# Performance work log

Measured on AMD Instinct MI355X. Metric: run time of the kernel, lower is better.

The kernel has to match this reference:

```python
import jax, jax.numpy as jnp
import numpy as np
from jax import lax

E = 3  # num_experts

def _maxpool2(x):
    return lax.reduce_window(x, -jnp.inf, lax.max, (1, 1, 2, 2), (1, 1, 2, 2), 'VALID')

def _mixed_conv(x, experts, routing, stride, pad):
    # per-sample expert-mixed convolution via grouped conv trick
    B, Ci, H, W = x.shape
    _, Co, _, k, _ = experts.shape
    kern = jnp.einsum('be,eoikl->boikl', routing, experts).reshape(B * Co, Ci, k, k)
    y = lax.conv_general_dilated(
        x.reshape(1, B * Ci, H, W), kern, (stride, stride),
        [(pad, pad), (pad, pad)],
        dimension_numbers=('NCHW', 'OIHW', 'NCHW'),
        feature_group_count=B)
    return y.reshape(B, Co, y.shape[2], y.shape[3])

def _dyres_conv(x, experts, rw, rb, stride=1, pad=1):
    # DyRes mode 'A': routing from avg-pool + spatial-std descriptors, softmax over experts
    avg = x.mean((2, 3))
    std = x.std((2, 3))
    r = jax.nn.softmax((avg + std) @ rw.T + rb, axis=-1)  # [B, E]
    return _mixed_conv(x, experts, r, stride, pad)

def _cond_conv(x, experts, rw, rb, stride=1, pad=1):
    # CondConv: sigmoid routing from global average pool
    r = jax.nn.sigmoid(x.mean((2, 3)) @ rw.T + rb)  # [B, E]
    return _mixed_conv(x, experts, r, stride, pad)

def _conv_init(key, co, ci, k):
    return jax.random.normal(key, (E, co, ci, k, k), jnp.float32) * np.sqrt(2.0 / (ci * k * k)).astype(np.float32)

def setup_inputs() -> dict:
    key = jax.random.key(0)
    ks = jax.random.split(key, 20)
    B = 512
    d = {}
    d['x'] = jax.random.normal(ks[0], (B, 3, 32, 32), jnp.float32)
    d['dw1'] = _conv_init(ks[1], 64, 3, 3)
    d['rw1'] = jax.random.normal(ks[2], (E, 3), jnp.float32) * 0.1
    d['rb1'] = jnp.zeros((E,), jnp.float32)
    d['dw2'] = _conv_init(ks[3], 192, 64, 3)
    d['rw2'] = jax.random.normal(ks[4], (E, 64), jnp.float32) * 0.1
    d['rb2'] = jnp.zeros((E,), jnp.float32)
    d['dw3'] = _conv_init(ks[5], 384, 192, 3)
    d['rw3'] = jax.random.normal(ks[6], (E, 192), jnp.float32) * 0.1
    d['rb3'] = jnp.zeros((E,), jnp.float32)
    d['cw4'] = _conv_init(ks[7], 256, 384, 3)
    d['cr4w'] = jax.random.normal(ks[8], (E, 384), jnp.float32) * 0.1
    d['cr4b'] = jnp.zeros((E,), jnp.float32)
    d['cw5'] = _conv_init(ks[9], 256, 256, 3)
    d['cr5w'] = jax.random.normal(ks[10], (E, 256), jnp.float32) * 0.1
    d['cr5b'] = jnp.zeros((E,), jnp.float32)
    d['fw1'] = jax.random.normal(ks[11], (4096, 1024), jnp.float32) * np.sqrt(2.0 / 1024).astype(np.float32)
    d['fb1'] = jnp.zeros((4096,), jnp.float32)
    d['fw2'] = jax.random.normal(ks[12], (4096, 4096), jnp.float32) * np.sqrt(2.0 / 4096).astype(np.float32)
    d['fb2'] = jnp.zeros((4096,), jnp.float32)
    d['fw3'] = jax.random.normal(ks[13], (100, 4096), jnp.float32) * np.sqrt(1.0 / 4096).astype(np.float32)
    d['fb3'] = jnp.zeros((100,), jnp.float32)
    return d

def reference(x, dw1, rw1, rb1, dw2, rw2, rb2, dw3, rw3, rb3,
              cw4, cr4w, cr4b, cw5, cr5w, cr5b,
              fw1, fb1, fw2, fb2, fw3, fb3):
    h = jax.nn.relu(_dyres_conv(x, dw1, rw1, rb1, stride=2))   # [B,64,16,16]
    h = _maxpool2(h)                                           # [B,64,8,8]
    h = jax.nn.relu(_dyres_conv(h, dw2, rw2, rb2))             # [B,192,8,8]
    h = _maxpool2(h)                                           # [B,192,4,4]
    h = jax.nn.relu(_dyres_conv(h, dw3, rw3, rb3))             # [B,384,4,4]
    h = jax.nn.relu(_cond_conv(h, cw4, cr4w, cr4b))            # [B,256,4,4]
    h = jax.nn.relu(_cond_conv(h, cw5, cr5w, cr5b))            # [B,256,4,4]
    h = _maxpool2(h)                                           # [B,256,2,2]
    h = h.reshape(h.shape[0], -1)                              # [B,1024]
    h = jax.nn.relu(h @ fw1.T + fb1)
    h = jax.nn.relu(h @ fw2.T + fb2)
    return h @ fw3.T + fb3                                     # [B,100]
```

## Files before the change

kernel.cpp:

```cpp
#include <hip/hip_runtime.h>
#include <math.h>


typedef unsigned short u16;
typedef unsigned int u32;
typedef short bf16x8 __attribute__((ext_vector_type(8)));
typedef float f32x4 __attribute__((ext_vector_type(4)));

__device__ __forceinline__ u16 bf16_rne(float f) {
    u32 u = __float_as_uint(f);
    return (u16)((u + 0x7fffu + ((u >> 16) & 1u)) >> 16);
}
__device__ __forceinline__ u32 packsplit(float v) {
    u16 h = bf16_rne(v);
    float hf = __uint_as_float((u32)h << 16);
    u16 l = bf16_rne(v - hf);
    return ((u32)h << 16) | l;
}
__device__ __forceinline__ float unpackf(u32 p) {
    return __uint_as_float(p & 0xffff0000u) + __uint_as_float(p << 16);
}
__device__ __forceinline__ int xcd_swz(int bid, int n) {
    if ((n & 7) != 0) return bid;
    int cpx = n >> 3;
    return (bid & 7) * cpx + (bid >> 3);
}

__global__ __launch_bounds__(256)
void wsplit_kernel(const float* __restrict__ W, u16* __restrict__ whi,
                   u16* __restrict__ wlo, int total, int Kper, int Kpad)
{
    int idx = blockIdx.x * 256 + threadIdx.x;
    if (idx >= total) return;
    int r = idx / Kpad, k = idx - r * Kpad;
    float v = (k < Kper) ? W[(size_t)r * Kper + k] : 0.f;
    u16 h = bf16_rne(v);
    whi[idx] = h;
    wlo[idx] = bf16_rne(v - __uint_as_float((u32)h << 16));
}

__global__ __launch_bounds__(256)
void wsplit_cl_kernel(const float* __restrict__ W, u16* __restrict__ whi,
                      u16* __restrict__ wlo, int total, int Ci)
{
    int idx = blockIdx.x * 256 + threadIdx.x;
    if (idx >= total) return;
    int Kper = 9 * Ci;
    int r = idx / Kper, kp = idx - r * Kper;
    int cell = kp / Ci, ci = kp - cell * Ci;
    float v = W[(size_t)r * Kper + ci * 9 + cell];
    u16 h = bf16_rne(v);
    whi[idx] = h;
    wlo[idx] = bf16_rne(v - __uint_as_float((u32)h << 16));
}

__global__ __launch_bounds__(64)
void stats_kernel(const float* __restrict__ actv, float* __restrict__ s,
                  int C, int HW, int use_std)
{
    int idx = blockIdx.x;
    size_t base = (size_t)idx * HW;
    int lane = threadIdx.x;
    float sum = 0.f, sq = 0.f;
    const float* p = actv + base;
    for (int i = lane; i < HW; i += 64) { float v = p[i]; sum += v; sq += v * v; }
#pragma unroll
    for (int off = 32; off > 0; off >>= 1) {
        sum += __shfl_down(sum, off);
        sq  += __shfl_down(sq, off);
    }
    if (lane == 0) {
        float inv = 1.f / (float)HW;
        float mean = sum * inv;
        float var = sq * inv - mean * mean;
        float outv = mean;
        if (use_std) outv += sqrtf(fmaxf(var, 0.f));
        s[idx] = outv;
    }
}

__global__ __launch_bounds__(384)
void stats_cl_kernel(const u32* __restrict__ act, float* __restrict__ s,
                     int H2, int W2, int C, int use_std)
{
    int b = blockIdx.x, c = threadIdx.x;
    int Hin = H2 - 2, Win = W2 - 2;
    float sum = 0.f, sq = 0.f;
    for (int h = 0; h < Hin; ++h)
        for (int w = 0; w < Win; ++w) {
            float v = unpackf(act[(((size_t)b * H2 + h + 1) * W2 + w + 1) * C + c]);
            sum += v; sq += v * v;
        }
    float inv = 1.f / (float)(Hin * Win);
    float mean = sum * inv;
    float var = sq * inv - mean * mean;
    float outv = mean;
    if (use_std) outv += sqrtf(fmaxf(var, 0.f));
    s[b * C + c] = outv;
}

__global__ __launch_bounds__(64)
void routing_kernel(const float* __restrict__ s, const float* __restrict__ rw,
                    const float* __restrict__ rb, float* __restrict__ r,
                    int C, int softmax_mode)
{
    int b = blockIdx.x;
    int lane = threadIdx.x;
    float d0 = 0.f, d1 = 0.f, d2 = 0.f;
    for (int c = lane; c < C; c += 64) {
        float sv = s[b * C + c];
        d0 += sv * rw[c];
        d1 += sv * rw[C + c];
        d2 += sv * rw[2 * C + c];
    }
#pragma unroll
    for (int off = 32; off > 0; off >>= 1) {
        d0 += __shfl_down(d0, off);
        d1 += __shfl_down(d1, off);
        d2 += __shfl_down(d2, off);
    }
    if (lane == 0) {
        d0 += rb[0]; d1 += rb[1]; d2 += rb[2];
        if (softmax_mode) {
            float mx = fmaxf(d0, fmaxf(d1, d2));
            float e0 = expf(d0 - mx), e1 = expf(d1 - mx), e2 = expf(d2 - mx);
            float inv = 1.f / (e0 + e1 + e2);
            r[b * 3 + 0] = e0 * inv;
            r[b * 3 + 1] = e1 * inv;
            r[b * 3 + 2] = e2 * inv;
        } else {
            r[b * 3 + 0] = 1.f / (1.f + expf(-d0));
            r[b * 3 + 1] = 1.f / (1.f + expf(-d1));
            r[b * 3 + 2] = 1.f / (1.f + expf(-d2));
        }
    }
}

template<int CI, int H2, int W2, int LGS, int LGOW>
__global__ __launch_bounds__(256, 2)
void cgemm_cl_kernel(const u16* __restrict__ Whi, const u16* __restrict__ Wlo,
                     const u32* __restrict__ Bpk, const float* __restrict__ rptr,
                     float* __restrict__ Cout, int M, int N, int Kper, int Kchunk)
{
    __shared__ __align__(16) u16 Ah[2][128 * 40], Al[2][128 * 40];
    __shared__ __align__(16) u16 Bh[2][128 * 40], Bl[2][128 * 40];
    const int tid = threadIdx.x;
    const int bx = xcd_swz(blockIdx.x, gridDim.x);
    const int n0 = bx << 7, m0 = blockIdx.y << 7;
    const int kq0 = blockIdx.z * Kchunk;

    const int rowA = tid >> 1, kh16 = (tid & 1) << 4;
    const int nB = tid & 127, kOff = (tid >> 7) << 4;

    const int nn = n0 + nB;
    const int bB = nn >> LGS;
    const int sidx = nn & ((1 << LGS) - 1);
    const int oh = sidx >> LGOW, ow = sidx & ((1 << LGOW) - 1);
    const long nBase = ((long)(bB * H2 + oh) * W2 + ow) * CI;

    const int lane = tid & 63, wv = tid >> 6;
    const int lm = lane & 15, qd = lane >> 4;
    const int wm = (wv & 1) << 6, wn = (wv >> 1) << 6;

    float rsv[3][4];
#pragma unroll
    for (int ni = 0; ni < 4; ++ni) {
        int n = n0 + wn + ni * 16 + lm;
        int b = n >> LGS;
#pragma unroll
        for (int e = 0; e < 3; ++e) rsv[e][ni] = rptr[b * 3 + e];
    }

    f32x4 acc[4][4], accS[4][4];
#pragma unroll
    for (int i = 0; i < 4; ++i)
#pragma unroll
        for (int j = 0; j < 4; ++j) {
            acc[i][j]  = (f32x4){0.f, 0.f, 0.f, 0.f};
            accS[i][j] = (f32x4){0.f, 0.f, 0.f, 0.f};
        }

    const int mg = m0 + rowA;
    const int nkz = Kchunk >> 5;
    const int NS = 3 * nkz;

    int eL = 0, kL = kq0;
    uint4 pA0, pA1, pA2, pA3;
    uint4 pQ0, pQ1, pQ2, pQ3;

    auto LOAD = [&]() {
        size_t aOff = ((size_t)(eL * M + mg)) * Kper + kL + kh16;
        const u16* hp = Whi + aOff;
        const u16* lp = Wlo + aOff;
        pA0 = *(const uint4*)hp; pA1 = *(const uint4*)(hp + 8);
        pA2 = *(const uint4*)lp; pA3 = *(const uint4*)(lp + 8);
        int k = kL + kOff;
        int cell = k / CI;
        int ci0 = k - cell * CI;
        int kh = (cell * 11) >> 5;
        int kw = cell - kh * 3;
        const u32* bp = Bpk + (nBase + (long)((kh * W2 + kw) * CI + ci0));
        pQ0 = *(const uint4*)bp;
        pQ1 = *(const uint4*)(bp + 4);
        pQ2 = *(const uint4*)(bp + 8);
        pQ3 = *(const uint4*)(bp + 12);
    };
    auto ADV = [&]() {
        kL += 32;
        if (kL == kq0 + Kchunk) { kL = kq0; ++eL; }
    };
    auto STORE = [&](int buf) {
        *(uint4*)(&Ah[buf][rowA * 40 + kh16])     = pA0;
        *(uint4*)(&Ah[buf][rowA * 40 + kh16 + 8]) = pA1;
        *(uint4*)(&Al[buf][rowA * 40 + kh16])     = pA2;
        *(uint4*)(&Al[buf][rowA * 40 + kh16 + 8]) = pA3;
        u32 qv[16] = {pQ0.x, pQ0.y, pQ0.z, pQ0.w, pQ1.x, pQ1.y, pQ1.z, pQ1.w,
                      pQ2.x, pQ2.y, pQ2.z, pQ2.w, pQ3.x, pQ3.y, pQ3.z, pQ3.w};
        u32 hw[8], lw[8];
#pragma unroll
        for (int j = 0; j < 8; ++j) {
            u32 p0 = qv[2 * j], p1 = qv[2 * j + 1];
            hw[j] = (p0 >> 16) | (p1 & 0xffff0000u);
            lw[j] = (p0 & 0xffffu) | (p1 << 16);
        }
        *(uint4*)(&Bh[buf][nB * 40 + kOff])     = make_uint4(hw[0], hw[1], hw[2], hw[3]);
        *(uint4*)(&Bh[buf][nB * 40 + kOff + 8]) = make_uint4(hw[4], hw[5], hw[6], hw[7]);
        *(uint4*)(&Bl[buf][nB * 40 + kOff])     = make_uint4(lw[0], lw[1], lw[2], lw[3]);
        *(uint4*)(&Bl[buf][nB * 40 + kOff + 8]) = make_uint4(lw[4], lw[5], lw[6], lw[7]);
    };
    auto COMPUTE = [&](int buf) {
        bf16x8 ah[4], al[4];
#pragma unroll
        for (int mi = 0; mi < 4; ++mi) {
            int row = wm + mi * 16 + lm;
            ah[mi] = *(const bf16x8*)(&Ah[buf][row * 40 + qd * 8]);
            al[mi] = *(const bf16x8*)(&Al[buf][row * 40 + qd * 8]);
        }
        __builtin_amdgcn_s_setprio(1);
#pragma unroll
        for (int ni = 0; ni < 4; ++ni) {
            int row = wn + ni * 16 + lm;
            bf16x8 bh = *(const bf16x8*)(&Bh[buf][row * 40 + qd * 8]);
            bf16x8 bl = *(const bf16x8*)(&Bl[buf][row * 40 + qd * 8]);
#pragma unroll
            for (int mi = 0; mi < 4; ++mi) {
                f32x4 c = acc[mi][ni];
                c = __builtin_amdgcn_mfma_f32_16x16x32_bf16(al[mi], bh, c, 0, 0, 0);
                c = __builtin_amdgcn_mfma_f32_16x16x32_bf16(ah[mi], bl, c, 0, 0, 0);
                c = __builtin_amdgcn_mfma_f32_16x16x32_bf16(ah[mi], bh, c, 0, 0, 0);
                acc[mi][ni] = c;
            }
        }
        __builtin_amdgcn_s_setprio(0);
    };

    LOAD(); ADV();
    int s = 0, buf = 0;
#pragma unroll
    for (int e = 0; e < 3; ++e) {
        for (int t = 0; t < nkz; ++t) {
            STORE(buf);
            if (s + 1 < NS) { LOAD(); ADV(); }
            asm volatile("s_waitcnt lgkmcnt(0)\n\ts_barrier" ::: "memory");
            COMPUTE(buf);
            buf ^= 1; ++s;
        }
#pragma unroll
        for (int mi = 0; mi < 4; ++mi)
#pragma unroll
            for (int ni = 0; ni < 4; ++ni) {
                accS[mi][ni] += acc[mi][ni] * rsv[e][ni];
                acc[mi][ni] = (f32x4){0.f, 0.f, 0.f, 0.f};
            }
    }

    const bool atom = (gridDim.z > 1);
#pragma unroll
    for (int ni = 0; ni < 4; ++ni) {
        int n = n0 + wn + ni * 16 + lm;
#pragma unroll
        for (int mi = 0; mi < 4; ++mi)
#pragma unroll
            for (int r = 0; r < 4; ++r) {
                int m = m0 + wm + mi * 16 + qd * 4 + r;
                if (m >= M) continue;
                float v = accS[mi][ni][r];
                if (atom) atomicAdd(&Cout[(size_t)n * M + m], v);
                else      Cout[(size_t)n * M + m] = v;
            }
    }
}

__global__ __launch_bounds__(256, 2)
void cgemm_l1_kernel(const u16* __restrict__ Whi, const u16* __restrict__ Wlo,
                     const u32* __restrict__ Bpk, const float* __restrict__ rptr,
                     float* __restrict__ Cout, int M, int N)
{
    __shared__ __align__(16) u16 Ah[2][128 * 40], Al[2][128 * 40];
    __shared__ __align__(16) u16 Bh[2][128 * 40], Bl[2][128 * 40];
    const int tid = threadIdx.x;
    const int bx = xcd_swz(blockIdx.x, gridDim.x);
    const int n0 = bx << 7;
    const int Kper = 27, Kpad = 32;
    const int H = 32, W = 32;

    const int rowA = tid >> 1, kh16 = (tid & 1) << 4;
    const int nB = tid & 127, kOff = (tid >> 7) << 4;

    const int nn = n0 + nB;
    const int bB = nn >> 8;
    const int sidx = nn & 255;
    const int ohs = (sidx >> 4) * 2 - 1;
    const int ows = (sidx & 15) * 2 - 1;
    const long nBase = (long)bB * 3072 + (long)ohs * W + ows;

    const int lane = tid & 63, wv = tid >> 6;
    const int lm = lane & 15, qd = lane >> 4;
    const int wm = (wv & 1) << 6, wn = (wv >> 1) << 6;

    float rsv[3][4];
#pragma unroll
    for (int ni = 0; ni < 4; ++ni) {
        int n = n0 + wn + ni * 16 + lm;
        int b = n >> 8;
#pragma unroll
        for (int e = 0; e < 3; ++e) rsv[e][ni] = rptr[b * 3 + e];
    }

    f32x4 acc[4][4], accS[4][4];
#pragma unroll
    for (int i = 0; i < 4; ++i)
#pragma unroll
        for (int j = 0; j < 4; ++j) {
            acc[i][j]  = (f32x4){0.f, 0.f, 0.f, 0.f};
            accS[i][j] = (f32x4){0.f, 0.f, 0.f, 0.f};
        }

    const int mg = rowA;
    int eL = 0;
    uint4 pA0, pA1, pA2, pA3;
    u32 pB[16];

    auto LOAD = [&]() {
        size_t aOff = ((size_t)(eL * M + mg)) * Kpad + kh16;
        const u16* hp = Whi + aOff;
        const u16* lp = Wlo + aOff;
        pA0 = *(const uint4*)hp; pA1 = *(const uint4*)(hp + 8);
        pA2 = *(const uint4*)lp; pA3 = *(const uint4*)(lp + 8);
#pragma unroll
        for (int j = 0; j < 16; ++j) {
            int k = kOff + j;
            int ci = (int)((unsigned)k / 9u);
            int r9 = k - ci * 9;
            int kh = (int)(((unsigned)r9 * 11u) >> 5);
            int kw = r9 - kh * 3;
            int ih = ohs + kh, iw = ows + kw;
            u32 p = 0;
            if (k < Kper && (unsigned)ih < (unsigned)H && (unsigned)iw < (unsigned)W)
                p = Bpk[nBase + (long)ci * 1024 + kh * W + kw];
            pB[j] = p;
        }
    };
    auto STORE = [&](int buf) {
        *(uint4*)(&Ah[buf][rowA * 40 + kh16])     = pA0;
        *(uint4*)(&Ah[buf][rowA * 40 + kh16 + 8]) = pA1;
        *(uint4*)(&Al[buf][rowA * 40 + kh16])     = pA2;
        *(uint4*)(&Al[buf][rowA * 40 + kh16 + 8]) = pA3;
        u32 hw[8], lw[8];
#pragma unroll
        for (int j = 0; j < 8; ++j) {
            u32 p0 = pB[2 * j], p1 = pB[2 * j + 1];
            hw[j] = (p0 >> 16) | (p1 & 0xffff0000u);
            lw[j] = (p0 & 0xffffu) | (p1 << 16);
        }
        *(uint4*)(&Bh[buf][nB * 40 + kOff])     = make_uint4(hw[0], hw[1], hw[2], hw[3]);
        *(uint4*)(&Bh[buf][nB * 40 + kOff + 8]) = make_uint4(hw[4], hw[5], hw[6], hw[7]);
        *(uint4*)(&Bl[buf][nB * 40 + kOff])     = make_uint4(lw[0], lw[1], lw[2], lw[3]);
        *(uint4*)(&Bl[buf][nB * 40 + kOff + 8]) = make_uint4(lw[4], lw[5], lw[6], lw[7]);
    };
    auto COMPUTE = [&](int buf) {
        bf16x8 ah[4], al[4];
#pragma unroll
        for (int mi = 0; mi < 4; ++mi) {
            int row = wm + mi * 16 + lm;
            ah[mi] = *(const bf16x8*)(&Ah[buf][row * 40 + qd * 8]);
            al[mi] = *(const bf16x8*)(&Al[buf][row * 40 + qd * 8]);
        }
        __builtin_amdgcn_s_setprio(1);
#pragma unroll
        for (int ni = 0; ni < 4; ++ni) {
            int row = wn + ni * 16 + lm;
            bf16x8 bh = *(const bf16x8*)(&Bh[buf][row * 40 + qd * 8]);
            bf16x8 bl = *(const bf16x8*)(&Bl[buf][row * 40 + qd * 8]);
#pragma unroll
            for (int mi = 0; mi < 4; ++mi) {
                f32x4 c = acc[mi][ni];
                c = __builtin_amdgcn_mfma_f32_16x16x32_bf16(al[mi], bh, c, 0, 0, 0);
                c = __builtin_amdgcn_mfma_f32_16x16x32_bf16(ah[mi], bl, c, 0, 0, 0);
                c = __builtin_amdgcn_mfma_f32_16x16x32_bf16(ah[mi], bh, c, 0, 0, 0);
                acc[mi][ni] = c;
            }
        }
        __builtin_amdgcn_s_setprio(0);
    };

    LOAD(); ++eL;
    int buf = 0;
#pragma unroll
    for (int e = 0; e < 3; ++e) {
        STORE(buf);
        if (e < 2) { LOAD(); ++eL; }
        asm volatile("s_waitcnt lgkmcnt(0)\n\ts_barrier" ::: "memory");
        COMPUTE(buf);
        buf ^= 1;
#pragma unroll
        for (int mi = 0; mi < 4; ++mi)
#pragma unroll
            for (int ni = 0; ni < 4; ++ni) {
                accS[mi][ni] += acc[mi][ni] * rsv[e][ni];
                acc[mi][ni] = (f32x4){0.f, 0.f, 0.f, 0.f};
            }
    }

#pragma unroll
    for (int ni = 0; ni < 4; ++ni) {
        int n = n0 + wn + ni * 16 + lm;
#pragma unroll
        for (int mi = 0; mi < 4; ++mi)
#pragma unroll
            for (int r = 0; r < 4; ++r) {
                int m = wm + mi * 16 + qd * 4 + r;
                if (m >= M) continue;
                Cout[(size_t)n * M + m] = accS[mi][ni][r];
            }
    }
}

template<int BIAS, int TROUT>
__global__ __launch_bounds__(256, 2)
void mgemm_kernel(const u16* __restrict__ Whi, const u16* __restrict__ Wlo,
                  const u32* __restrict__ Bpk, const float* __restrict__ bias,
                  float* __restrict__ Cout,
                  int M, int N, int Kpad, int Kchunk)
{
    __shared__ __align__(16) u16 Ah[2][128 * 40], Al[2][128 * 40];
    __shared__ __align__(16) u32 Bp[2][128 * 36];
    const int tid = threadIdx.x;
    const int n0 = blockIdx.x << 7, m0 = blockIdx.y << 7;
    const int bz = blockIdx.z;
    const int kq0 = bz * Kchunk;
    const int kEnd = kq0 + Kchunk;

    const int rowA = tid >> 1, kh16 = (tid & 1) << 4;
    const int nB = tid & 127, kOff = (tid >> 7) << 4;

    const int lane = tid & 63, wv = tid >> 6;
    const int lm = lane & 15, qd = lane >> 4;
    const int wm = (wv & 1) << 6, wn = (wv >> 1) << 6;

    f32x4 acc[4][4];
#pragma unroll
    for (int i = 0; i < 4; ++i)
#pragma unroll
        for (int j = 0; j < 4; ++j)
            acc[i][j] = (f32x4){0.f, 0.f, 0.f, 0.f};

    const int mg = m0 + rowA;
    uint4 pA0, pA1, pA2, pA3;
    uint4 pQ0, pQ1, pQ2, pQ3;

    auto LOAD = [&](int kq) {
        if (mg < M) {
            const u16* hp = Whi + (size_t)mg * Kpad + kq + kh16;
            const u16* lp = Wlo + (size_t)mg * Kpad + kq + kh16;
            pA0 = *(const uint4*)hp; pA1 = *(const uint4*)(hp + 8);
            pA2 = *(const uint4*)lp; pA3 = *(const uint4*)(lp + 8);
        } else {
            pA0 = make_uint4(0,0,0,0); pA1 = make_uint4(0,0,0,0);
            pA2 = make_uint4(0,0,0,0); pA3 = make_uint4(0,0,0,0);
        }
        const u32* bp = Bpk + (size_t)(n0 + nB) * Kpad + kq + kOff;
        pQ0 = *(const uint4*)bp;
        pQ1 = *(const uint4*)(bp + 4);
        pQ2 = *(const uint4*)(bp + 8);
        pQ3 = *(const uint4*)(bp + 12);
    };
    auto STORE = [&](int buf) {
        *(uint4*)(&Ah[buf][rowA * 40 + kh16])     = pA0;
        *(uint4*)(&Ah[buf][rowA * 40 + kh16 + 8]) = pA1;
        *(uint4*)(&Al[buf][rowA * 40 + kh16])     = pA2;
        *(uint4*)(&Al[buf][rowA * 40 + kh16 + 8]) = pA3;
        u32* bp = &Bp[buf][nB * 36 + kOff];
        *(uint4*)(bp)      = pQ0;
        *(uint4*)(bp + 4)  = pQ1;
        *(uint4*)(bp + 8)  = pQ2;
        *(uint4*)(bp + 12) = pQ3;
    };
    auto COMPUTE = [&](int buf) {
        bf16x8 ah[4], al[4];
#pragma unroll
        for (int mi = 0; mi < 4; ++mi) {
            int row = wm + mi * 16 + lm;
            ah[mi] = *(const bf16x8*)(&Ah[buf][row * 40 + qd * 8]);
            al[mi] = *(const bf16x8*)(&Al[buf][row * 40 + qd * 8]);
        }
        __builtin_amdgcn_s_setprio(1);
#pragma unroll
        for (int ni = 0; ni < 4; ++ni) {
            const u32* bp = &Bp[buf][(wn + ni * 16 + lm) * 36 + qd * 8];
            uint4 p0 = *(const uint4*)bp;
            uint4 p1 = *(const uint4*)(bp + 4);
            union { u32 w[4]; bf16x8 v; } bh, bl;
            bh.w[0] = (p0.x >> 16) | (p0.y & 0xffff0000u);
            bl.w[0] = (p0.x & 0xffffu) | (p0.y << 16);
            bh.w[1] = (p0.z >> 16) | (p0.w & 0xffff0000u);
            bl.w[1] = (p0.z & 0xffffu) | (p0.w << 16);
            bh.w[2] = (p1.x >> 16) | (p1.y & 0xffff0000u);
            bl.w[2] = (p1.x & 0xffffu) | (p1.y << 16);
            bh.w[3] = (p1.z >> 16) | (p1.w & 0xffff0000u);
            bl.w[3] = (p1.z & 0xffffu) | (p1.w << 16);
#pragma unroll
            for (int mi = 0; mi < 4; ++mi) {
                f32x4 c = acc[mi][ni];
                c = __builtin_amdgcn_mfma_f32_16x16x32_bf16(al[mi], bh.v, c, 0, 0, 0);
                c = __builtin_amdgcn_mfma_f32_16x16x32_bf16(ah[mi], bl.v, c, 0, 0, 0);
                c = __builtin_amdgcn_mfma_f32_16x16x32_bf16(ah[mi], bh.v, c, 0, 0, 0);
                acc[mi][ni] = c;
            }
        }
        __builtin_amdgcn_s_setprio(0);
    };

    LOAD(kq0);
    int buf = 0;
    for (int kq = kq0; kq < kEnd; kq += 32) {
        STORE(buf);
        if (kq + 32 < kEnd) LOAD(kq + 32);
        asm volatile("s_waitcnt lgkmcnt(0)\n\ts_barrier" ::: "memory");
        COMPUTE(buf);
        buf ^= 1;
    }

#pragma unroll
    for (int ni = 0; ni < 4; ++ni) {
        int n = n0 + wn + ni * 16 + lm;
        if (n >= N) continue;
#pragma unroll
        for (int mi = 0; mi < 4; ++mi)
#pragma unroll
            for (int r = 0; r < 4; ++r) {
                int m = m0 + wm + mi * 16 + qd * 4 + r;
                if (m >= M) continue;
                float v = acc[mi][ni][r];
                if (BIAS && bz == 0) v += bias[m];
                if (TROUT) atomicAdd(&Cout[(size_t)n * M + m], v);
                else       atomicAdd(&Cout[(size_t)m * N + n], v);
            }
    }
}

__global__ __launch_bounds__(256)
void pack_kernel(const float* __restrict__ in, u32* __restrict__ outp, int count)
{
    int i = blockIdx.x * 256 + threadIdx.x;
    if (i >= count) return;
    outp[i] = packsplit(in[i]);
}

__global__ __launch_bounds__(256)
void pool_pack_cl_kernel(const float* __restrict__ in, u32* __restrict__ outp,
                         int Bn, int Hin, int Win, int C)
{
    int OH = Hin >> 1, OW = Win >> 1, H2 = OH + 2, W2 = OW + 2;
    int total = Bn * H2 * W2 * C;
    int i = blockIdx.x * 256 + threadIdx.x;
    if (i >= total) return;
    int c = i % C; int t = i / C;
    int w = t % W2; t /= W2;
    int h = t % H2; int b = t / H2;
    u32 pv = 0;
    if (h >= 1 && h <= OH && w >= 1 && w <= OW) {
        int oh = h - 1, ow = w - 1;
        const float* p = in + (((size_t)b * Hin + 2 * oh) * Win + 2 * ow) * C + c;
        size_t rs = (size_t)Win * C;
        float v = fmaxf(fmaxf(p[0], p[C]), fmaxf(p[rs], p[rs + C]));
        pv = packsplit(fmaxf(v, 0.f));
    }
    outp[i] = pv;
}

__global__ __launch_bounds__(256)
void pack_cl_kernel(const float* __restrict__ in, u32* __restrict__ outp,
                    int Bn, int Hin, int Win, int C)
{
    int H2 = Hin + 2, W2 = Win + 2;
    int total = Bn * H2 * W2 * C;
    int i = blockIdx.x * 256 + threadIdx.x;
    if (i >= total) return;
    int c = i % C; int t = i / C;
    int w = t % W2; t /= W2;
    int h = t % H2; int b = t / H2;
    u32 pv = 0;
    if (h >= 1 && h <= Hin && w >= 1 && w <= Win) {
        float v = in[(((size_t)b * Hin + (h - 1)) * Win + (w - 1)) * C + c];
        pv = packsplit(fmaxf(v, 0.f));
    }
    outp[i] = pv;
}

__global__ __launch_bounds__(256)
void pool_flatten_cl_kernel(const float* __restrict__ in, u32* __restrict__ outp)
{
    int i = blockIdx.x * 256 + threadIdx.x;
    if (i >= 512 * 1024) return;
    int b = i >> 10;
    int f = i & 1023;
    int c = f >> 2, sp = f & 3;
    int oh = sp >> 1, ow = sp & 1;
    const float* p = in + (((size_t)b * 4 + 2 * oh) * 4 + 2 * ow) * 256 + c;
    float v = fmaxf(fmaxf(p[0], p[256]), fmaxf(p[1024], p[1024 + 256]));
    outp[i] = packsplit(fmaxf(v, 0.f));
}

__global__ __launch_bounds__(256)
void tp_pack_kernel(const float* __restrict__ in, u32* __restrict__ outp,
                    int Mt, int Nt)
{
    __shared__ float t[32][33];
    int tx = threadIdx.x & 31, ty = threadIdx.x >> 5;
    int mB = blockIdx.x << 5, nB = blockIdx.y << 5;
#pragma unroll
    for (int i = 0; i < 4; ++i) {
        int mm = ty + i * 8;
        t[mm][tx] = in[(size_t)(mB + mm) * Nt + nB + tx];
    }
    __syncthreads();
#pragma unroll
    for (int i = 0; i < 4; ++i) {
        int nn = ty + i * 8;
        float v = fmaxf(t[tx][nn], 0.f);
        outp[(size_t)(nB + nn) * Mt + mB + tx] = packsplit(v);
    }
}

extern "C" void kernel_launch(void* const* d_in, const int* in_sizes, int n_in,
                              void* d_out, int out_size, void* d_ws, size_t ws_size,
                              hipStream_t stream)
{
    const float* x    = (const float*)d_in[0];
    const float* dw1  = (const float*)d_in[1];
    const float* rw1  = (const float*)d_in[2];
    const float* rb1  = (const float*)d_in[3];
    const float* dw2  = (const float*)d_in[4];
    const float* rw2  = (const float*)d_in[5];
    const float* rb2  = (const float*)d_in[6];
    const float* dw3  = (const float*)d_in[7];
    const float* rw3  = (const float*)d_in[8];
    const float* rb3  = (const float*)d_in[9];
    const float* cw4  = (const float*)d_in[10];
    const float* cr4w = (const float*)d_in[11];
    const float* cr4b = (const float*)d_in[12];
    const float* cw5  = (const float*)d_in[13];
    const float* cr5w = (const float*)d_in[14];
    const float* cr5b = (const float*)d_in[15];
    const float* fw1  = (const float*)d_in[16];
    const float* fb1  = (const float*)d_in[17];
    const float* fw2  = (const float*)d_in[18];
    const float* fb2  = (const float*)d_in[19];
    const float* fw3  = (const float*)d_in[20];
    const float* fb3  = (const float*)d_in[21];
    float* out = (float*)d_out;

    float* ws    = (float*)d_ws;
    float* r1    = ws;
    float* r2    = r1 + 1536;
    float* r3    = r2 + 1536;
    float* r4    = r3 + 1536;
    float* r5    = r4 + 1536;
    float* sdesc = ws + 8192 + 65536;
    const size_t REGION = 18874368;
    float* region = sdesc + 196608;
    float* slab   = region;
    u32*   a3u    = (u32*)(region + 4194304);
    u16*   regEnd = (u16*)(region + REGION);
    u32*   P1     = (u32*)(region + REGION);

    u16 *w1h = regEnd - 2*(size_t)6144,     *w1l = regEnd - (size_t)6144;
    u16 *w2h = regEnd - 2*(size_t)331776,   *w2l = regEnd - (size_t)331776;
    u16 *w3h = regEnd - 2*(size_t)1990656,  *w3l = regEnd - (size_t)1990656;
    u16 *w4h = regEnd - 2*(size_t)2654208,  *w4l = regEnd - (size_t)2654208;
    u16 *w5h = regEnd - 2*(size_t)1769472,  *w5l = regEnd - (size_t)1769472;
    u16 *f1h = regEnd - 2*(size_t)4194304,  *f1l = regEnd - (size_t)4194304;
    u16 *f2h = regEnd - 2*(size_t)16777216, *f2l = regEnd - (size_t)16777216;
    u16 *f3h = regEnd - 2*(size_t)409600,   *f3l = regEnd - (size_t)409600;

    u32* xpk   = P1;
    u32* a1    = P1;
    u32* a2    = P1;
    u32* a4    = P1;
    u32* hTpk  = P1;
    u32* f1pkT = P1 + 1048576;
    u32* f2pkT = P1 + 3145728;

    const int B = 512;

    pack_kernel<<<6144, 256, 0, stream>>>(x, xpk, 1572864);

    wsplit_kernel<<<24, 256, 0, stream>>>(dw1, w1h, w1l, 6144, 27, 32);
    stats_kernel<<<B * 3, 64, 0, stream>>>(x, sdesc, 3, 1024, 1);
    routing_kernel<<<B, 64, 0, stream>>>(sdesc, rw1, rb1, r1, 3, 1);
    cgemm_l1_kernel<<<dim3(1024, 1, 1), 256, 0, stream>>>(
        w1h, w1l, xpk, r1, slab, 64, 131072);
    pool_pack_cl_kernel<<<12800, 256, 0, stream>>>(slab, a1, B, 16, 16, 64);

    wsplit_cl_kernel<<<1296, 256, 0, stream>>>(dw2, w2h, w2l, 331776, 64);
    stats_cl_kernel<<<B, 64, 0, stream>>>(a1, sdesc, 10, 10, 64, 1);
    routing_kernel<<<B, 64, 0, stream>>>(sdesc, rw2, rb2, r2, 64, 1);
    cgemm_cl_kernel<64, 10, 10, 6, 3><<<dim3(256, 2, 1), 256, 0, stream>>>(
        w2h, w2l, a1, r2, slab, 192, 32768, 576, 576);
    pool_pack_cl_kernel<<<13824, 256, 0, stream>>>(slab, a2, B, 8, 8, 192);

    wsplit_cl_kernel<<<7776, 256, 0, stream>>>(dw3, w3h, w3l, 1990656, 192);
    stats_cl_kernel<<<B, 192, 0, stream>>>(a2, sdesc, 6, 6, 192, 1);
    routing_kernel<<<B, 64, 0, stream>>>(sdesc, rw3, rb3, r3, 192, 1);
    hipMemsetAsync(slab, 0, (size_t)8192 * 384 * 4, stream);
    cgemm_cl_kernel<192, 6, 6, 4, 2><<<dim3(64, 3, 2), 256, 0, stream>>>(
        w3h, w3l, a2, r3, slab, 384, 8192, 1728, 864);
    pack_cl_kernel<<<27648, 256, 0, stream>>>(slab, a3u, B, 4, 4, 384);

    wsplit_cl_kernel<<<10368, 256, 0, stream>>>(cw4, w4h, w4l, 2654208, 384);
    stats_cl_kernel<<<B, 384, 0, stream>>>(a3u, sdesc, 6, 6, 384, 0);
    routing_kernel<<<B, 64, 0, stream>>>(sdesc, cr4w, cr4b, r4, 384, 0);
    hipMemsetAsync(slab, 0, (size_t)8192 * 256 * 4, stream);
    cgemm_cl_kernel<384, 6, 6, 4, 2><<<dim3(64, 2, 4), 256, 0, stream>>>(
        w4h, w4l, a3u, r4, slab, 256, 8192, 3456, 864);
    pack_cl_kernel<<<18432, 256, 0, stream>>>(slab, a4, B, 4, 4, 256);

    wsplit_cl_kernel<<<6912, 256, 0, stream>>>(cw5, w5h, w5l, 1769472, 256);
    stats_cl_kernel<<<B, 256, 0, stream>>>(a4, sdesc, 6, 6, 256, 0);
    routing_kernel<<<B, 64, 0, stream>>>(sdesc, cr5w, cr5b, r5, 256, 0);
    hipMemsetAsync(slab, 0, (size_t)8192 * 256 * 4, stream);
    cgemm_cl_kernel<256, 6, 6, 4, 2><<<dim3(64, 2, 4), 256, 0, stream>>>(
        w5h, w5l, a4, r5, slab, 256, 8192, 2304, 576);

    pool_flatten_cl_kernel<<<2048, 256, 0, stream>>>(slab, hTpk);

    wsplit_kernel<<<16384, 256, 0, stream>>>(fw1, f1h, f1l, 4194304, 1024, 1024);
    hipMemsetAsync(slab, 0, (size_t)4096 * 512 * 4, stream);
    mgemm_kernel<1, 0><<<dim3(4, 32, 8), 256, 0, stream>>>(
        f1h, f1l, hTpk, fb1, slab, 4096, 512, 1024, 128);
    tp_pack_kernel<<<dim3(128, 16), 256, 0, stream>>>(slab, f1pkT, 4096, 512);

    wsplit_kernel<<<65536, 256, 0, stream>>>(fw2, f2h, f2l, 16777216, 4096, 4096);
    hipMemsetAsync(slab, 0, (size_t)4096 * 512 * 4, stream);
    mgemm_kernel<1, 0><<<dim3(4, 32, 8), 256, 0, stream>>>(
        f2h, f2l, f1pkT, fb2, slab, 4096, 512, 4096, 512);
    tp_pack_kernel<<<dim3(128, 16), 256, 0, stream>>>(slab, f2pkT, 4096, 512);

    wsplit_kernel<<<1600, 256, 0, stream>>>(fw3, f3h, f3l, 409600, 4096, 4096);
    hipMemsetAsync(out, 0, (size_t)512 * 100 * 4, stream);
    mgemm_kernel<1, 1><<<dim3(4, 1, 32), 256, 0, stream>>>(
        f3h, f3l, f2pkT, fb3, out, 100, 512, 4096, 128);
}
```

Before: 1.486 ms.

## Add 256x256-tile 512-thread expert-mixed conv GEMM with packed hi/lo weights

```diff
diff --git a/kernel.cpp b/kernel.cpp
--- a/kernel.cpp
+++ b/kernel.cpp
@@ -52,6 +52,22 @@
     u16 h = bf16_rne(v);
     whi[idx] = h;
     wlo[idx] = bf16_rne(v - __uint_as_float((u32)h << 16));
+}
+
+__global__ __launch_bounds__(256)
+void wsplit_clp_kernel(const float* __restrict__ W, u32* __restrict__ wp,
+                       int total, int Ci, int Kpad)
+{
+    int idx = blockIdx.x * 256 + threadIdx.x;
+    if (idx >= total) return;
+    int Kper = 9 * Ci;
+    int r = idx / Kpad, k = idx - r * Kpad;
+    u32 p = 0;
+    if (k < Kper) {
+        int cell = k / Ci, ci = k - cell * Ci;
+        p = packsplit(W[(size_t)r * Kper + ci * 9 + cell]);
+    }
+    wp[idx] = p;
 }
 
 __global__ __launch_bounds__(64)
@@ -133,6 +149,174 @@
             r[b * 3 + 1] = 1.f / (1.f + expf(-d1));
             r[b * 3 + 2] = 1.f / (1.f + expf(-d2));
         }
+    }
+}
+
+template<int CI, int H2, int W2, int LGS, int LGOW>
+__global__ __launch_bounds__(512, 2)
+void cgemm8_kernel(const u32* __restrict__ Apk, const u32* __restrict__ Bpk,
+                   const float* __restrict__ rptr, float* __restrict__ Cout,
+                   int M, int N, int Kper, int Kpad, int Kchunk)
+{
+    __shared__ __align__(16) u32 ApS[2][256 * 36];
+    __shared__ __align__(16) u32 BpS[2][256 * 36];
+    const int tid = threadIdx.x;
+    const int bx = xcd_swz(blockIdx.x, gridDim.x);
+    const int n0 = bx << 8, m0 = blockIdx.y << 8;
+    const int kq0 = blockIdx.z * Kchunk;
+
+    const int rowA = tid >> 1, ka16 = (tid & 1) << 4;
+    const int nB = tid & 255, kb16 = (tid >> 8) << 4;
+
+    const int nn = n0 + nB;
+    const int bB = nn >> LGS;
+    const int sidx = nn & ((1 << LGS) - 1);
+    const int oh = sidx >> LGOW, ow = sidx & ((1 << LGOW) - 1);
+    const long nBase = ((long)(bB * H2 + oh) * W2 + ow) * CI;
+    const float rv0 = rptr[bB * 3 + 0];
+    const float rv1 = rptr[bB * 3 + 1];
+    const float rv2 = rptr[bB * 3 + 2];
+
+    const int lane = tid & 63, wv = tid >> 6;
+    const int lm = lane & 15, qd = lane >> 4;
+    const int wm = (wv & 3) << 6, wn = (wv >> 2) << 7;
+
+    f32x4 acc[4][8];
+#pragma unroll
+    for (int i = 0; i < 4; ++i)
+#pragma unroll
+        for (int j = 0; j < 8; ++j)
+            acc[i][j] = (f32x4){0.f, 0.f, 0.f, 0.f};
+
+    uint4 pA0, pA1, pA2, pA3;
+    uint4 pQ0, pQ1, pQ2, pQ3;
+
+    auto LOAD_A = [&](int e, int k) {
+        const u32* ap = Apk + ((size_t)(e * M + m0 + rowA)) * Kpad + k + ka16;
+        pA0 = *(const uint4*)ap;
+        pA1 = *(const uint4*)(ap + 4);
+        pA2 = *(const uint4*)(ap + 8);
+        pA3 = *(const uint4*)(ap + 12);
+    };
+    auto LOAD_B = [&](int k) {
+        int kb = k + kb16;
+        if (kb < Kper) {
+            int cell = kb / CI;
+            int ci0 = kb - cell * CI;
+            int kh = (cell * 11) >> 5;
+            int kw = cell - kh * 3;
+            const u32* bp = Bpk + (nBase + (long)((kh * W2 + kw) * CI + ci0));
+            pQ0 = *(const uint4*)bp;
+            pQ1 = *(const uint4*)(bp + 4);
+            pQ2 = *(const uint4*)(bp + 8);
+            pQ3 = *(const uint4*)(bp + 12);
+        } else {
+            pQ0 = make_uint4(0,0,0,0); pQ1 = make_uint4(0,0,0,0);
+            pQ2 = make_uint4(0,0,0,0); pQ3 = make_uint4(0,0,0,0);
+        }
+    };
+    auto STORE_A = [&](int buf) {
+        u32* ap = &ApS[buf][rowA * 36 + ka16];
+        *(uint4*)(ap)      = pA0;
+        *(uint4*)(ap + 4)  = pA1;
+        *(uint4*)(ap + 8)  = pA2;
+        *(uint4*)(ap + 12) = pA3;
+    };
+    auto STORE_B = [&](int buf, float r) {
+        u32 qv[16] = {pQ0.x, pQ0.y, pQ0.z, pQ0.w, pQ1.x, pQ1.y, pQ1.z, pQ1.w,
+                      pQ2.x, pQ2.y, pQ2.z, pQ2.w, pQ3.x, pQ3.y, pQ3.z, pQ3.w};
+        u32 sv[16];
+#pragma unroll
+        for (int j = 0; j < 16; ++j)
+            sv[j] = packsplit(unpackf(qv[j]) * r);
+        u32* bp = &BpS[buf][nB * 36 + kb16];
+        *(uint4*)(bp)      = make_uint4(sv[0], sv[1], sv[2], sv[3]);
+        *(uint4*)(bp + 4)  = make_uint4(sv[4], sv[5], sv[6], sv[7]);
+        *(uint4*)(bp + 8)  = make_uint4(sv[8], sv[9], sv[10], sv[11]);
+        *(uint4*)(bp + 12) = make_uint4(sv[12], sv[13], sv[14], sv[15]);
+    };
+    auto COMPUTE = [&](int buf) {
+        bf16x8 ah[4], al[4];
+#pragma unroll
+        for (int mi = 0; mi < 4; ++mi) {
+            const u32* ap = &ApS[buf][(wm + mi * 16 + lm) * 36 + qd * 8];
+            uint4 q0 = *(const uint4*)ap;
+            uint4 q1 = *(const uint4*)(ap + 4);
+            union { u32 w[4]; bf16x8 v; } h, l;
+            h.w[0] = (q0.x >> 16) | (q0.y & 0xffff0000u);
+            l.w[0] = (q0.x & 0xffffu) | (q0.y << 16);
+            h.w[1] = (q0.z >> 16) | (q0.w & 0xffff0000u);
+            l.w[1] = (q0.z & 0xffffu) | (q0.w << 16);
+            h.w[2] = (q1.x >> 16) | (q1.y & 0xffff0000u);
+            l.w[2] = (q1.x & 0xffffu) | (q1.y << 16);
+            h.w[3] = (q1.z >> 16) | (q1.w & 0xffff0000u);
+            l.w[3] = (q1.z & 0xffffu) | (q1.w << 16);
+            ah[mi] = h.v; al[mi] = l.v;
+        }
+        __builtin_amdgcn_s_setprio(1);
+#pragma unroll
+        for (int ni = 0; ni < 8; ++ni) {
+            const u32* bp = &BpS[buf][(wn + ni * 16 + lm) * 36 + qd * 8];
+            uint4 p0 = *(const uint4*)bp;
+            uint4 p1 = *(const uint4*)(bp + 4);
+            union { u32 w[4]; bf16x8 v; } bh, bl;
+            bh.w[0] = (p0.x >> 16) | (p0.y & 0xffff0000u);
+            bl.w[0] = (p0.x & 0xffffu) | (p0.y << 16);
+            bh.w[1] = (p0.z >> 16) | (p0.w & 0xffff0000u);
+            bl.w[1] = (p0.z & 0xffffu) | (p0.w << 16);
+            bh.w[2] = (p1.x >> 16) | (p1.y & 0xffff0000u);
+            bl.w[2] = (p1.x & 0xffffu) | (p1.y << 16);
+            bh.w[3] = (p1.z >> 16) | (p1.w & 0xffff0000u);
+            bl.w[3] = (p1.z & 0xffffu) | (p1.w << 16);
+#pragma unroll
+            for (int mi = 0; mi < 4; ++mi) {
+                f32x4 c = acc[mi][ni];
+                c = __builtin_amdgcn_mfma_f32_16x16x32_bf16(al[mi], bh.v, c, 0, 0, 0);
+                c = __builtin_amdgcn_mfma_f32_16x16x32_bf16(ah[mi], bl.v, c, 0, 0, 0);
+                c = __builtin_amdgcn_mfma_f32_16x16x32_bf16(ah[mi], bh.v, c, 0, 0, 0);
+                acc[mi][ni] = c;
+            }
+        }
+        __builtin_amdgcn_s_setprio(0);
+    };
+
+    const int nkz = Kchunk >> 5;
+    LOAD_B(kq0);
+    LOAD_A(0, kq0);
+    int buf = 0;
+    for (int t = 0; t < nkz; ++t) {
+        int k = kq0 + (t << 5);
+        STORE_A(buf);
+        STORE_B(buf, rv0);
+        LOAD_A(1, k);
+        asm volatile("s_waitcnt lgkmcnt(0)\n\ts_barrier" ::: "memory");
+        COMPUTE(buf);
+        buf ^= 1;
+        STORE_A(buf);
+        STORE_B(buf, rv1);
+        LOAD_A(2, k);
+        asm volatile("s_waitcnt lgkmcnt(0)\n\ts_barrier" ::: "memory");
+        COMPUTE(buf);
+        buf ^= 1;
+        STORE_A(buf);
+        STORE_B(buf, rv2);
+        if (t + 1 < nkz) { LOAD_A(0, k + 32); LOAD_B(k + 32); }
+        asm volatile("s_waitcnt lgkmcnt(0)\n\ts_barrier" ::: "memory");
+        COMPUTE(buf);
+        buf ^= 1;
+    }
+
+#pragma unroll
+    for (int ni = 0; ni < 8; ++ni) {
+        int n = n0 + wn + ni * 16 + lm;
+#pragma unroll
+        for (int mi = 0; mi < 4; ++mi)
+#pragma unroll
+            for (int r = 0; r < 4; ++r) {
+                int m = m0 + wm + mi * 16 + qd * 4 + r;
+                if (m >= M) continue;
+                atomicAdd(&Cout[(size_t)n * M + m], acc[mi][ni][r]);
+            }
     }
 }
 
@@ -683,16 +867,18 @@
     float* slab   = region;
     u32*   a3u    = (u32*)(region + 4194304);
     u16*   regEnd = (u16*)(region + REGION);
+    u32*   regEndU = (u32*)(region + REGION);
     u32*   P1     = (u32*)(region + REGION);
 
     u16 *w1h = regEnd - 2*(size_t)6144,     *w1l = regEnd - (size_t)6144;
-    u16 *w2h = regEnd - 2*(size_t)331776,   *w2l = regEnd - (size_t)331776;
     u16 *w3h = regEnd - 2*(size_t)1990656,  *w3l = regEnd - (size_t)1990656;
-    u16 *w4h = regEnd - 2*(size_t)2654208,  *w4l = regEnd - (size_t)2654208;
-    u16 *w5h = regEnd - 2*(size_t)1769472,  *w5l = regEnd - (size_t)1769472;
     u16 *f1h = regEnd - 2*(size_t)4194304,  *f1l = regEnd - (size_t)4194304;
     u16 *f2h = regEnd - 2*(size_t)16777216, *f2l = regEnd - (size_t)16777216;
     u16 *f3h = regEnd - 2*(size_t)409600,   *f3l = regEnd - (size_t)409600;
+
+    u32 *w2p = regEndU - (size_t)331776;
+    u32 *w4p = regEndU - (size_t)2752512;
+    u32 *w5p = regEndU - (size_t)1769472;
 
     u32* xpk   = P1;
     u32* a1    = P1;
@@ -713,11 +899,12 @@
         w1h, w1l, xpk, r1, slab, 64, 131072);
     pool_pack_cl_kernel<<<12800, 256, 0, stream>>>(slab, a1, B, 16, 16, 64);
 
-    wsplit_cl_kernel<<<1296, 256, 0, stream>>>(dw2, w2h, w2l, 331776, 64);
+    wsplit_clp_kernel<<<1296, 256, 0, stream>>>(dw2, w2p, 331776, 64, 576);
     stats_cl_kernel<<<B, 64, 0, stream>>>(a1, sdesc, 10, 10, 64, 1);
     routing_kernel<<<B, 64, 0, stream>>>(sdesc, rw2, rb2, r2, 64, 1);
-    cgemm_cl_kernel<64, 10, 10, 6, 3><<<dim3(256, 2, 1), 256, 0, stream>>>(
-        w2h, w2l, a1, r2, slab, 192, 32768, 576, 576);
+    hipMemsetAsync(slab, 0, (size_t)192 * 32768 * 4, stream);
+    cgemm8_kernel<64, 10, 10, 6, 3><<<dim3(128, 1, 2), 512, 0, stream>>>(
+        w2p, a1, r2, slab, 192, 32768, 576, 576, 288);
     pool_pack_cl_kernel<<<13824, 256, 0, stream>>>(slab, a2, B, 8, 8, 192);
 
     wsplit_cl_kernel<<<7776, 256, 0, stream>>>(dw3, w3h, w3l, 1990656, 192);
@@ -728,20 +915,20 @@
         w3h, w3l, a2, r3, slab, 384, 8192, 1728, 864);
     pack_cl_kernel<<<27648, 256, 0, stream>>>(slab, a3u, B, 4, 4, 384);
 
-    wsplit_cl_kernel<<<10368, 256, 0, stream>>>(cw4, w4h, w4l, 2654208, 384);
+    wsplit_clp_kernel<<<10752, 256, 0, stream>>>(cw4, w4p, 2752512, 384, 3584);
     stats_cl_kernel<<<B, 384, 0, stream>>>(a3u, sdesc, 6, 6, 384, 0);
     routing_kernel<<<B, 64, 0, stream>>>(sdesc, cr4w, cr4b, r4, 384, 0);
     hipMemsetAsync(slab, 0, (size_t)8192 * 256 * 4, stream);
-    cgemm_cl_kernel<384, 6, 6, 4, 2><<<dim3(64, 2, 4), 256, 0, stream>>>(
-        w4h, w4l, a3u, r4, slab, 256, 8192, 3456, 864);
+    cgemm8_kernel<384, 6, 6, 4, 2><<<dim3(32, 1, 8), 512, 0, stream>>>(
+        w4p, a3u, r4, slab, 256, 8192, 3456, 3584, 448);
     pack_cl_kernel<<<18432, 256, 0, stream>>>(slab, a4, B, 4, 4, 256);
 
-    wsplit_cl_kernel<<<6912, 256, 0, stream>>>(cw5, w5h, w5l, 1769472, 256);
+    wsplit_clp_kernel<<<6912, 256, 0, stream>>>(cw5, w5p, 1769472, 256, 2304);
     stats_cl_kernel<<<B, 256, 0, stream>>>(a4, sdesc, 6, 6, 256, 0);
     routing_kernel<<<B, 64, 0, stream>>>(sdesc, cr5w, cr5b, r5, 256, 0);
     hipMemsetAsync(slab, 0, (size_t)8192 * 256 * 4, stream);
-    cgemm_cl_kernel<256, 6, 6, 4, 2><<<dim3(64, 2, 4), 256, 0, stream>>>(
-        w5h, w5l, a4, r5, slab, 256, 8192, 2304, 576);
+    cgemm8_kernel<256, 6, 6, 4, 2><<<dim3(32, 1, 8), 512, 0, stream>>>(
+        w5p, a4, r5, slab, 256, 8192, 2304, 2304, 288);
 
     pool_flatten_cl_kernel<<<2048, 256, 0, stream>>>(slab, hTpk);
 
```

New measurement: 1.830 ms. 1.23x slower.

## Halve K-tile in conv GEMM, fold routing scale into B, raise split-K

Applied to the files above, without the earlier changes.

```diff
diff --git a/kernel.cpp b/kernel.cpp
--- a/kernel.cpp
+++ b/kernel.cpp
@@ -5,6 +5,7 @@
 typedef unsigned short u16;
 typedef unsigned int u32;
 typedef short bf16x8 __attribute__((ext_vector_type(8)));
+typedef short bf16x4 __attribute__((ext_vector_type(4)));
 typedef float f32x4 __attribute__((ext_vector_type(4)));
 
 __device__ __forceinline__ u16 bf16_rne(float f) {
@@ -25,6 +26,18 @@
     int cpx = n >> 3;
     return (bid & 7) * cpx + (bid >> 3);
 }
+
+#if __has_builtin(__builtin_amdgcn_mfma_f32_16x16x16bf16_1k)
+__device__ __forceinline__ f32x4 mfma16(bf16x4 a, bf16x4 b, f32x4 c) {
+    return __builtin_amdgcn_mfma_f32_16x16x16bf16_1k(a, b, c, 0, 0, 0);
+}
+#else
+__device__ __forceinline__ f32x4 mfma16(bf16x4 a, bf16x4 b, f32x4 c) {
+    bf16x8 az = {a[0], a[1], a[2], a[3], (short)0, (short)0, (short)0, (short)0};
+    bf16x8 bz = {b[0], b[1], b[2], b[3], (short)0, (short)0, (short)0, (short)0};
+    return __builtin_amdgcn_mfma_f32_16x16x32_bf16(az, bz, c, 0, 0, 0);
+}
+#endif
 
 __global__ __launch_bounds__(256)
 void wsplit_kernel(const float* __restrict__ W, u16* __restrict__ whi,
@@ -137,64 +150,54 @@
 }
 
 template<int CI, int H2, int W2, int LGS, int LGOW>
-__global__ __launch_bounds__(256, 2)
+__global__ __launch_bounds__(256, 3)
 void cgemm_cl_kernel(const u16* __restrict__ Whi, const u16* __restrict__ Wlo,
                      const u32* __restrict__ Bpk, const float* __restrict__ rptr,
                      float* __restrict__ Cout, int M, int N, int Kper, int Kchunk)
 {
-    __shared__ __align__(16) u16 Ah[2][128 * 40], Al[2][128 * 40];
-    __shared__ __align__(16) u16 Bh[2][128 * 40], Bl[2][128 * 40];
+    __shared__ __align__(16) u16 Ah[2][128 * 20], Al[2][128 * 20];
+    __shared__ __align__(16) u16 Bh[2][128 * 20], Bl[2][128 * 20];
     const int tid = threadIdx.x;
     const int bx = xcd_swz(blockIdx.x, gridDim.x);
     const int n0 = bx << 7, m0 = blockIdx.y << 7;
     const int kq0 = blockIdx.z * Kchunk;
 
-    const int rowA = tid >> 1, kh16 = (tid & 1) << 4;
-    const int nB = tid & 127, kOff = (tid >> 7) << 4;
-
-    const int nn = n0 + nB;
+    const int rowA = tid >> 1, kh8 = (tid & 1) << 3;
+    const int nBr = tid >> 1, kOffB = (tid & 1) << 3;
+
+    const int nn = n0 + nBr;
     const int bB = nn >> LGS;
     const int sidx = nn & ((1 << LGS) - 1);
     const int oh = sidx >> LGOW, ow = sidx & ((1 << LGOW) - 1);
     const long nBase = ((long)(bB * H2 + oh) * W2 + ow) * CI;
+    const float rsB0 = rptr[bB * 3 + 0];
+    const float rsB1 = rptr[bB * 3 + 1];
+    const float rsB2 = rptr[bB * 3 + 2];
 
     const int lane = tid & 63, wv = tid >> 6;
     const int lm = lane & 15, qd = lane >> 4;
     const int wm = (wv & 1) << 6, wn = (wv >> 1) << 6;
 
-    float rsv[3][4];
-#pragma unroll
-    for (int ni = 0; ni < 4; ++ni) {
-        int n = n0 + wn + ni * 16 + lm;
-        int b = n >> LGS;
-#pragma unroll
-        for (int e = 0; e < 3; ++e) rsv[e][ni] = rptr[b * 3 + e];
-    }
-
-    f32x4 acc[4][4], accS[4][4];
+    f32x4 acc[4][4];
 #pragma unroll
     for (int i = 0; i < 4; ++i)
 #pragma unroll
-        for (int j = 0; j < 4; ++j) {
-            acc[i][j]  = (f32x4){0.f, 0.f, 0.f, 0.f};
-            accS[i][j] = (f32x4){0.f, 0.f, 0.f, 0.f};
-        }
+        for (int j = 0; j < 4; ++j)
+            acc[i][j] = (f32x4){0.f, 0.f, 0.f, 0.f};
 
     const int mg = m0 + rowA;
-    const int nkz = Kchunk >> 5;
+    const int nkz = Kchunk >> 4;
     const int NS = 3 * nkz;
 
     int eL = 0, kL = kq0;
-    uint4 pA0, pA1, pA2, pA3;
-    uint4 pQ0, pQ1, pQ2, pQ3;
+    uint4 pAh, pAl;
+    uint4 pQ0, pQ1;
 
     auto LOAD = [&]() {
-        size_t aOff = ((size_t)(eL * M + mg)) * Kper + kL + kh16;
-        const u16* hp = Whi + aOff;
-        const u16* lp = Wlo + aOff;
-        pA0 = *(const uint4*)hp; pA1 = *(const uint4*)(hp + 8);
-        pA2 = *(const uint4*)lp; pA3 = *(const uint4*)(lp + 8);
-        int k = kL + kOff;
+        size_t aOff = ((size_t)(eL * M + mg)) * Kper + kL + kh8;
+        pAh = *(const uint4*)(Whi + aOff);
+        pAl = *(const uint4*)(Wlo + aOff);
+        int k = kL + kOffB;
         int cell = k / CI;
         int ci0 = k - cell * CI;
         int kh = (cell * 11) >> 5;
@@ -202,52 +205,49 @@
         const u32* bp = Bpk + (nBase + (long)((kh * W2 + kw) * CI + ci0));
         pQ0 = *(const uint4*)bp;
         pQ1 = *(const uint4*)(bp + 4);
-        pQ2 = *(const uint4*)(bp + 8);
-        pQ3 = *(const uint4*)(bp + 12);
     };
     auto ADV = [&]() {
-        kL += 32;
+        kL += 16;
         if (kL == kq0 + Kchunk) { kL = kq0; ++eL; }
     };
-    auto STORE = [&](int buf) {
-        *(uint4*)(&Ah[buf][rowA * 40 + kh16])     = pA0;
-        *(uint4*)(&Ah[buf][rowA * 40 + kh16 + 8]) = pA1;
-        *(uint4*)(&Al[buf][rowA * 40 + kh16])     = pA2;
-        *(uint4*)(&Al[buf][rowA * 40 + kh16 + 8]) = pA3;
-        u32 qv[16] = {pQ0.x, pQ0.y, pQ0.z, pQ0.w, pQ1.x, pQ1.y, pQ1.z, pQ1.w,
-                      pQ2.x, pQ2.y, pQ2.z, pQ2.w, pQ3.x, pQ3.y, pQ3.z, pQ3.w};
-        u32 hw[8], lw[8];
-#pragma unroll
-        for (int j = 0; j < 8; ++j) {
-            u32 p0 = qv[2 * j], p1 = qv[2 * j + 1];
+    auto STORE = [&](int buf, float rs) {
+        *(uint4*)(&Ah[buf][rowA * 20 + kh8]) = pAh;
+        *(uint4*)(&Al[buf][rowA * 20 + kh8]) = pAl;
+        u32 qv[8] = {pQ0.x, pQ0.y, pQ0.z, pQ0.w, pQ1.x, pQ1.y, pQ1.z, pQ1.w};
+        u32 sv[8];
+#pragma unroll
+        for (int j = 0; j < 8; ++j)
+            sv[j] = packsplit(unpackf(qv[j]) * rs);
+        u32 hw[4], lw[4];
+#pragma unroll
+        for (int j = 0; j < 4; ++j) {
+            u32 p0 = sv[2 * j], p1 = sv[2 * j + 1];
             hw[j] = (p0 >> 16) | (p1 & 0xffff0000u);
             lw[j] = (p0 & 0xffffu) | (p1 << 16);
         }
-        *(uint4*)(&Bh[buf][nB * 40 + kOff])     = make_uint4(hw[0], hw[1], hw[2], hw[3]);
-        *(uint4*)(&Bh[buf][nB * 40 + kOff + 8]) = make_uint4(hw[4], hw[5], hw[6], hw[7]);
-        *(uint4*)(&Bl[buf][nB * 40 + kOff])     = make_uint4(lw[0], lw[1], lw[2], lw[3]);
-        *(uint4*)(&Bl[buf][nB * 40 + kOff + 8]) = make_uint4(lw[4], lw[5], lw[6], lw[7]);
+        *(uint4*)(&Bh[buf][nBr * 20 + kOffB]) = make_uint4(hw[0], hw[1], hw[2], hw[3]);
+        *(uint4*)(&Bl[buf][nBr * 20 + kOffB]) = make_uint4(lw[0], lw[1], lw[2], lw[3]);
     };
     auto COMPUTE = [&](int buf) {
-        bf16x8 ah[4], al[4];
+        bf16x4 ah[4], al[4];
 #pragma unroll
         for (int mi = 0; mi < 4; ++mi) {
-            int row = wm + mi * 16 + lm;
-            ah[mi] = *(const bf16x8*)(&Ah[buf][row * 40 + qd * 8]);
-            al[mi] = *(const bf16x8*)(&Al[buf][row * 40 + qd * 8]);
+            int off = (wm + mi * 16 + lm) * 20 + qd * 4;
+            ah[mi] = *(const bf16x4*)(&Ah[buf][off]);
+            al[mi] = *(const bf16x4*)(&Al[buf][off]);
         }
         __builtin_amdgcn_s_setprio(1);
 #pragma unroll
         for (int ni = 0; ni < 4; ++ni) {
-            int row = wn + ni * 16 + lm;
-            bf16x8 bh = *(const bf16x8*)(&Bh[buf][row * 40 + qd * 8]);
-            bf16x8 bl = *(const bf16x8*)(&Bl[buf][row * 40 + qd * 8]);
+            int off = (wn + ni * 16 + lm) * 20 + qd * 4;
+            bf16x4 bh = *(const bf16x4*)(&Bh[buf][off]);
+            bf16x4 bl = *(const bf16x4*)(&Bl[buf][off]);
 #pragma unroll
             for (int mi = 0; mi < 4; ++mi) {
                 f32x4 c = acc[mi][ni];
-                c = __builtin_amdgcn_mfma_f32_16x16x32_bf16(al[mi], bh, c, 0, 0, 0);
-                c = __builtin_amdgcn_mfma_f32_16x16x32_bf16(ah[mi], bl, c, 0, 0, 0);
-                c = __builtin_amdgcn_mfma_f32_16x16x32_bf16(ah[mi], bh, c, 0, 0, 0);
+                c = mfma16(al[mi], bh, c);
+                c = mfma16(ah[mi], bl, c);
+                c = mfma16(ah[mi], bh, c);
                 acc[mi][ni] = c;
             }
         }
@@ -258,20 +258,14 @@
     int s = 0, buf = 0;
 #pragma unroll
     for (int e = 0; e < 3; ++e) {
+        const float rs = (e == 0) ? rsB0 : ((e == 1) ? rsB1 : rsB2);
         for (int t = 0; t < nkz; ++t) {
-            STORE(buf);
+            STORE(buf, rs);
             if (s + 1 < NS) { LOAD(); ADV(); }
             asm volatile("s_waitcnt lgkmcnt(0)\n\ts_barrier" ::: "memory");
             COMPUTE(buf);
             buf ^= 1; ++s;
         }
-#pragma unroll
-        for (int mi = 0; mi < 4; ++mi)
-#pragma unroll
-            for (int ni = 0; ni < 4; ++ni) {
-                accS[mi][ni] += acc[mi][ni] * rsv[e][ni];
-                acc[mi][ni] = (f32x4){0.f, 0.f, 0.f, 0.f};
-            }
     }
 
     const bool atom = (gridDim.z > 1);
@@ -284,7 +278,7 @@
             for (int r = 0; r < 4; ++r) {
                 int m = m0 + wm + mi * 16 + qd * 4 + r;
                 if (m >= M) continue;
-                float v = accS[mi][ni][r];
+                float v = acc[mi][ni][r];
                 if (atom) atomicAdd(&Cout[(size_t)n * M + m], v);
                 else      Cout[(size_t)n * M + m] = v;
             }
@@ -716,32 +710,33 @@
     wsplit_cl_kernel<<<1296, 256, 0, stream>>>(dw2, w2h, w2l, 331776, 64);
     stats_cl_kernel<<<B, 64, 0, stream>>>(a1, sdesc, 10, 10, 64, 1);
     routing_kernel<<<B, 64, 0, stream>>>(sdesc, rw2, rb2, r2, 64, 1);
-    cgemm_cl_kernel<64, 10, 10, 6, 3><<<dim3(256, 2, 1), 256, 0, stream>>>(
-        w2h, w2l, a1, r2, slab, 192, 32768, 576, 576);
+    hipMemsetAsync(slab, 0, (size_t)192 * 32768 * 4, stream);
+    cgemm_cl_kernel<64, 10, 10, 6, 3><<<dim3(256, 2, 2), 256, 0, stream>>>(
+        w2h, w2l, a1, r2, slab, 192, 32768, 576, 288);
     pool_pack_cl_kernel<<<13824, 256, 0, stream>>>(slab, a2, B, 8, 8, 192);
 
     wsplit_cl_kernel<<<7776, 256, 0, stream>>>(dw3, w3h, w3l, 1990656, 192);
     stats_cl_kernel<<<B, 192, 0, stream>>>(a2, sdesc, 6, 6, 192, 1);
     routing_kernel<<<B, 64, 0, stream>>>(sdesc, rw3, rb3, r3, 192, 1);
     hipMemsetAsync(slab, 0, (size_t)8192 * 384 * 4, stream);
-    cgemm_cl_kernel<192, 6, 6, 4, 2><<<dim3(64, 3, 2), 256, 0, stream>>>(
-        w3h, w3l, a2, r3, slab, 384, 8192, 1728, 864);
+    cgemm_cl_kernel<192, 6, 6, 4, 2><<<dim3(64, 3, 4), 256, 0, stream>>>(
+        w3h, w3l, a2, r3, slab, 384, 8192, 1728, 432);
     pack_cl_kernel<<<27648, 256, 0, stream>>>(slab, a3u, B, 4, 4, 384);
 
     wsplit_cl_kernel<<<10368, 256, 0, stream>>>(cw4, w4h, w4l, 2654208, 384);
     stats_cl_kernel<<<B, 384, 0, stream>>>(a3u, sdesc, 6, 6, 384, 0);
     routing_kernel<<<B, 64, 0, stream>>>(sdesc, cr4w, cr4b, r4, 384, 0);
     hipMemsetAsync(slab, 0, (size_t)8192 * 256 * 4, stream);
-    cgemm_cl_kernel<384, 6, 6, 4, 2><<<dim3(64, 2, 4), 256, 0, stream>>>(
-        w4h, w4l, a3u, r4, slab, 256, 8192, 3456, 864);
+    cgemm_cl_kernel<384, 6, 6, 4, 2><<<dim3(64, 2, 6), 256, 0, stream>>>(
+        w4h, w4l, a3u, r4, slab, 256, 8192, 3456, 576);
     pack_cl_kernel<<<18432, 256, 0, stream>>>(slab, a4, B, 4, 4, 256);
 
     wsplit_cl_kernel<<<6912, 256, 0, stream>>>(cw5, w5h, w5l, 1769472, 256);
     stats_cl_kernel<<<B, 256, 0, stream>>>(a4, sdesc, 6, 6, 256, 0);
     routing_kernel<<<B, 64, 0, stream>>>(sdesc, cr5w, cr5b, r5, 256, 0);
     hipMemsetAsync(slab, 0, (size_t)8192 * 256 * 4, stream);
-    cgemm_cl_kernel<256, 6, 6, 4, 2><<<dim3(64, 2, 4), 256, 0, stream>>>(
-        w5h, w5l, a4, r5, slab, 256, 8192, 2304, 576);
+    cgemm_cl_kernel<256, 6, 6, 4, 2><<<dim3(64, 2, 6), 256, 0, stream>>>(
+        w5h, w5l, a4, r5, slab, 256, 8192, 2304, 384);
 
     pool_flatten_cl_kernel<<<2048, 256, 0, stream>>>(slab, hTpk);
 
```

After: 1.807 ms. 21.7% more time.
